# Kernel tuning notes

Measured on AMD Instinct MI355X. Metric: run time of the kernel, lower is better.

Reference implementation:

```python
import jax, jax.numpy as jnp
import numpy as np

N = 8192
IN_F = 512
OUT_F = 64
ALPHA = 0.2  # LeakyReLU negative slope
NEG_INF = -9e15


def setup_inputs() -> dict:
    key = jax.random.key(0)
    k1, k2, k3, k4 = jax.random.split(key, 4)
    x = jax.random.normal(k1, (N, IN_F), dtype=jnp.float32)
    adj = jax.random.randint(k2, (N, N), 0, 2, dtype=jnp.int32)
    # xavier_uniform with gain=1.414
    def xavier(k, shape, gain=1.414):
        fan_in, fan_out = shape[0], shape[1]
        a = gain * np.sqrt(6.0 / (fan_in + fan_out))
        return jax.random.uniform(k, shape, jnp.float32, -a, a)
    W = xavier(k3, (IN_F, OUT_F))
    a = xavier(k4, (2 * OUT_F, 1))
    return {"x": x, "adj": adj, "W": W, "a": a}


def reference(x, adj, W, a):
    h = x @ W  # [N, F]
    f = W.shape[1]
    # e[i,j] = leakyrelu([h_i, h_j] @ a) = leakyrelu(h_i@a1 + h_j@a2)
    e1 = h @ a[:f, 0]   # [N]
    e2 = h @ a[f:, 0]   # [N]
    e = jax.nn.leaky_relu(e1[:, None] + e2[None, :], negative_slope=ALPHA)  # [N, N]
    scores = jnp.where(adj > 0, e, NEG_INF)
    attention = jax.nn.softmax(scores, axis=1)  # dropout p=0.0 -> identity
    h_prime = attention @ h  # [N, F]
    return jax.nn.elu(h_prime)  # concat=True
```

## Files before the change

kernel.cpp:

```cpp
#include <hip/hip_runtime.h>
#include <hip/hip_bf16.h>

#define NN 8192
#define KF 512
#define FF 64
#define GAT_ALPHA 0.2f
#define MSHIFT 20.0f
#define LOG2E 1.44269504f

#define JSPLIT 16
#define JW (NN / JSPLIT)
#define KSTEPS (JW / 32)

#define EXP2F(x) __builtin_amdgcn_exp2f(x)

typedef __attribute__((ext_vector_type(8))) __bf16 bf16x8;
typedef __attribute__((ext_vector_type(4))) float f32x4;
typedef __attribute__((ext_vector_type(4))) int   i32x4;

__global__ __launch_bounds__(256) void gat_linear(
    const float* __restrict__ x, const float* __restrict__ W,
    const float* __restrict__ av, __hip_bfloat16* __restrict__ ht,
    float* __restrict__ e1, float* __restrict__ e2)
{
    __shared__ float xs[32][33];
    __shared__ float Ws[32][64];
    __shared__ float ep[2][32][17];

    const int t  = threadIdx.x;
    const int fq = t & 15;
    const int rq = t >> 4;
    const int i0 = blockIdx.x * 32;

    const int kl = t & 31, r0 = t >> 5;
    const int fw = t & 63, kq = t >> 6;

    float acc[2][4] = {};

    for (int kt = 0; kt < KF; kt += 32) {
        #pragma unroll
        for (int m = 0; m < 4; ++m)
            xs[kl][r0 + 8 * m] = x[(size_t)(i0 + r0 + 8 * m) * KF + kt + kl];
        #pragma unroll
        for (int m = 0; m < 8; ++m)
            Ws[kq + 4 * m][fw] = W[(size_t)(kt + kq + 4 * m) * FF + fw];
        __syncthreads();
        #pragma unroll
        for (int kk = 0; kk < 32; ++kk) {
            float x0 = xs[kk][rq * 2];
            float x1 = xs[kk][rq * 2 + 1];
            f32x4 wv = *(const f32x4*)&Ws[kk][fq * 4];
            #pragma unroll
            for (int v = 0; v < 4; ++v) {
                acc[0][v] += x0 * wv[v];
                acc[1][v] += x1 * wv[v];
            }
        }
        __syncthreads();
    }

    #pragma unroll
    for (int v = 0; v < 4; ++v) {
        int f = fq * 4 + v;
        union { ushort2 q; __hip_bfloat16 h[2]; } pk;
        pk.h[0] = __float2bfloat16(acc[0][v]);
        pk.h[1] = __float2bfloat16(acc[1][v]);
        *(ushort2*)&ht[(size_t)f * NN + i0 + rq * 2] = pk.q;
    }

    f32x4 a1v = *(const f32x4*)&av[fq * 4];
    f32x4 a2v = *(const f32x4*)&av[64 + fq * 4];
    #pragma unroll
    for (int u = 0; u < 2; ++u) {
        float s1 = 0.f, s2 = 0.f;
        #pragma unroll
        for (int v = 0; v < 4; ++v) {
            s1 += acc[u][v] * a1v[v];
            s2 += acc[u][v] * a2v[v];
        }
        ep[0][rq * 2 + u][fq] = s1;
        ep[1][rq * 2 + u][fq] = s2;
    }
    __syncthreads();
    if (t < 32) {
        float s1 = 0.f, s2 = 0.f;
        #pragma unroll
        for (int q = 0; q < 16; ++q) { s1 += ep[0][t][q]; s2 += ep[1][t][q]; }
        e1[i0 + t] = s1 * LOG2E;
        e2[i0 + t] = s2 * LOG2E;
    }
}

__global__ __launch_bounds__(256, 4) void gat_attn(
    const int* __restrict__ adj, const __hip_bfloat16* __restrict__ ht,
    const float* __restrict__ e1, const float* __restrict__ e2,
    float* __restrict__ accs, float* __restrict__ lsums)
{
    const int t     = threadIdx.x;
    const int lane  = t & 63;
    const int wv    = t >> 6;
    const int n16   = lane & 15;
    const int quad  = lane >> 4;
    const int split = blockIdx.x & (JSPLIT - 1);
    const int i0    = (blockIdx.x >> 4) * 64 + wv * 16;
    const int j0    = split * JW;
    const int row   = i0 + n16;

    const float e1L = e1[row];
    float ms = e1L + MSHIFT * LOG2E;
    const float miL = ms > 0.f ? ms : GAT_ALPHA * ms;
    const float c0  = e1L - miL;
    const float c1  = GAT_ALPHA * e1L - miL;

    const int*            ap  = adj + (size_t)row * NN + j0 + quad * 8;
    const float*          epx = e2 + j0 + quad * 8;
    const __hip_bfloat16* hp  = ht + (size_t)n16 * NN + j0 + quad * 8;

    i32x4  aA[2][2];
    float4 eA[2][2];
    f32x4 dacc[4] = {{0.f,0.f,0.f,0.f},{0.f,0.f,0.f,0.f},{0.f,0.f,0.f,0.f},{0.f,0.f,0.f,0.f}};
    f32x4 dl = {0.f, 0.f, 0.f, 0.f};

    union { unsigned short s[8]; bf16x8 v; } ones;
    #pragma unroll
    for (int k = 0; k < 8; ++k) ones.s[k] = 0x3F80;

#define LOADA(sl, st)                                                          \
    {                                                                          \
        aA[sl][0] = *(const i32x4*)(ap + (st) * 32);                           \
        aA[sl][1] = *(const i32x4*)(ap + (st) * 32 + 4);                       \
    }
#define LOADE(sl, st)                                                          \
    {                                                                          \
        eA[sl][0] = *(const float4*)(epx + (st) * 32);                         \
        eA[sl][1] = *(const float4*)(epx + (st) * 32 + 4);                     \
    }

    LOADA(0, 0) LOADA(1, 1)
    LOADE(0, 0) LOADE(1, 1)

    #pragma unroll
    for (int st = 0; st < KSTEPS; ++st) {
        const int sl = st & 1;

        bf16x8 b0 = *(const bf16x8*)(hp + (size_t)st * 32);
        bf16x8 b1 = *(const bf16x8*)(hp + (size_t)16 * NN + st * 32);
        bf16x8 b2 = *(const bf16x8*)(hp + (size_t)32 * NN + st * 32);
        bf16x8 b3 = *(const bf16x8*)(hp + (size_t)48 * NN + st * 32);

        i32x4  a0 = aA[sl][0], a1 = aA[sl][1];
        float4 e0 = eA[sl][0], ev = eA[sl][1];
        if (st + 2 < KSTEPS) { LOADA(sl, st + 2) LOADE(sl, st + 2) }

        union { bf16x8 v; __hip_bfloat16 h[8]; } af;
#define PJ(idx, aval, eval)                                                    \
        {                                                                      \
            float t0 = c0 + (eval);                                            \
            float t1 = __builtin_fmaf(GAT_ALPHA, (eval), c1);                  \
            float p_ = EXP2F(fmaxf(t0, t1));                                   \
            af.h[idx] = __float2bfloat16((aval) > 0 ? p_ : 0.f);               \
        }
        PJ(0, a0.x, e0.x) PJ(1, a0.y, e0.y) PJ(2, a0.z, e0.z) PJ(3, a0.w, e0.w)
        PJ(4, a1.x, ev.x) PJ(5, a1.y, ev.y) PJ(6, a1.z, ev.z) PJ(7, a1.w, ev.w)
#undef PJ

        dacc[0] = __builtin_amdgcn_mfma_f32_16x16x32_bf16(af.v, b0, dacc[0], 0, 0, 0);
        dacc[1] = __builtin_amdgcn_mfma_f32_16x16x32_bf16(af.v, b1, dacc[1], 0, 0, 0);
        dacc[2] = __builtin_amdgcn_mfma_f32_16x16x32_bf16(af.v, b2, dacc[2], 0, 0, 0);
        dacc[3] = __builtin_amdgcn_mfma_f32_16x16x32_bf16(af.v, b3, dacc[3], 0, 0, 0);
        dl      = __builtin_amdgcn_mfma_f32_16x16x32_bf16(af.v, ones.v, dl, 0, 0, 0);
    }
#undef LOADA
#undef LOADE

    if (n16 == 0) {
        #pragma unroll
        for (int r = 0; r < 4; ++r)
            lsums[(size_t)split * NN + i0 + quad * 4 + r] = dl[r];
    }

    float* ab = accs + (size_t)split * NN * FF;
    #pragma unroll
    for (int ft = 0; ft < 4; ++ft)
        #pragma unroll
        for (int r = 0; r < 4; ++r)
            ab[(size_t)(i0 + quad * 4 + r) * FF + ft * 16 + n16] = dacc[ft][r];
}

__global__ __launch_bounds__(256) void gat_epilogue(
    const float* __restrict__ accs, const float* __restrict__ lsums,
    float* __restrict__ out)
{
    const int idx = (blockIdx.x * 256 + threadIdx.x) * 4;
    const int row = idx >> 6;

    float l = 0.f;
    #pragma unroll
    for (int s = 0; s < JSPLIT; ++s) l += lsums[(size_t)s * NN + row];

    f32x4 a = {0.f, 0.f, 0.f, 0.f};
    #pragma unroll
    for (int s = 0; s < JSPLIT; ++s) {
        f32x4 v = *(const f32x4*)(accs + (size_t)s * NN * FF + idx);
        a.x += v.x; a.y += v.y; a.z += v.z; a.w += v.w;
    }

    const float li = 1.f / l;
    f32x4 o;
    #pragma unroll
    for (int v = 0; v < 4; ++v) {
        float hv = a[v] * li;
        o[v] = hv > 0.f ? hv : __expf(hv) - 1.f;
    }
    *(f32x4*)(out + idx) = o;
}

extern "C" void kernel_launch(void* const* d_in, const int* in_sizes, int n_in,
                              void* d_out, int out_size, void* d_ws, size_t ws_size,
                              hipStream_t stream) {
    const float* x   = (const float*)d_in[0];
    const int*   adj = (const int*)d_in[1];
    const float* W   = (const float*)d_in[2];
    const float* av  = (const float*)d_in[3];
    float* out = (float*)d_out;

    char* wsb = (char*)d_ws;
    __hip_bfloat16* ht = (__hip_bfloat16*)wsb;
    float* e1    = (float*)(wsb + (1 << 20));
    float* e2    = e1 + NN;
    float* accs  = e2 + NN;
    float* lsums = accs + (size_t)JSPLIT * NN * FF;

    gat_linear<<<256, 256, 0, stream>>>(x, W, av, ht, e1, e2);
    gat_attn<<<(NN / 64) * JSPLIT, 256, 0, stream>>>(adj, ht, e1, e2, accs, lsums);
    gat_epilogue<<<NN * FF / 1024, 256, 0, stream>>>(accs, lsums, out);
}
```

Baseline: 432.2 us.

## Pre-pack adjacency into a bitmask in a separate kernel and halve the column split

```diff
diff --git a/kernel.cpp b/kernel.cpp
--- a/kernel.cpp
+++ b/kernel.cpp
@@ -8,7 +8,7 @@
 #define MSHIFT 20.0f
 #define LOG2E 1.44269504f
 
-#define JSPLIT 16
+#define JSPLIT 8
 #define JW (NN / JSPLIT)
 #define KSTEPS (JW / 32)
 
@@ -16,7 +16,35 @@
 
 typedef __attribute__((ext_vector_type(8))) __bf16 bf16x8;
 typedef __attribute__((ext_vector_type(4))) float f32x4;
-typedef __attribute__((ext_vector_type(4))) int   i32x4;
+
+__global__ __launch_bounds__(256) void adj_compress(
+    const int* __restrict__ adj, unsigned* __restrict__ mask)
+{
+    const int b   = blockIdx.x * 256 + threadIdx.x;
+    const int st4 =  b       & 7;
+    const int q   = (b >> 3) & 3;
+    const int s   = (b >> 5) & 7;
+    const int row =  b >> 8;
+
+    const int* ap = adj + (size_t)row * NN + s * JW + q * 8;
+    unsigned w = 0;
+    #pragma unroll
+    for (int k = 0; k < 4; ++k) {
+        const int st = st4 * 4 + k;
+        int4 a0 = *(const int4*)(ap + st * 32);
+        int4 a1 = *(const int4*)(ap + st * 32 + 4);
+        unsigned by =  (unsigned)(a0.x > 0)
+                    | ((unsigned)(a0.y > 0) << 1)
+                    | ((unsigned)(a0.z > 0) << 2)
+                    | ((unsigned)(a0.w > 0) << 3)
+                    | ((unsigned)(a1.x > 0) << 4)
+                    | ((unsigned)(a1.y > 0) << 5)
+                    | ((unsigned)(a1.z > 0) << 6)
+                    | ((unsigned)(a1.w > 0) << 7);
+        w |= by << (8 * k);
+    }
+    mask[b] = w;
+}
 
 __global__ __launch_bounds__(256) void gat_linear(
     const float* __restrict__ x, const float* __restrict__ W,
@@ -92,7 +120,7 @@
 }
 
 __global__ __launch_bounds__(256, 4) void gat_attn(
-    const int* __restrict__ adj, const __hip_bfloat16* __restrict__ ht,
+    const unsigned short* __restrict__ maskh, const __hip_bfloat16* __restrict__ ht,
     const float* __restrict__ e1, const float* __restrict__ e2,
     float* __restrict__ accs, float* __restrict__ lsums)
 {
@@ -102,7 +130,7 @@
     const int n16   = lane & 15;
     const int quad  = lane >> 4;
     const int split = blockIdx.x & (JSPLIT - 1);
-    const int i0    = (blockIdx.x >> 4) * 64 + wv * 16;
+    const int i0    = (blockIdx.x >> 3) * 64 + wv * 16;
     const int j0    = split * JW;
     const int row   = i0 + n16;
 
@@ -112,12 +140,10 @@
     const float c0  = e1L - miL;
     const float c1  = GAT_ALPHA * e1L - miL;
 
-    const int*            ap  = adj + (size_t)row * NN + j0 + quad * 8;
+    const unsigned short* mp = maskh + (size_t)row * 512 + split * 64 + quad * 16;
     const float*          epx = e2 + j0 + quad * 8;
     const __hip_bfloat16* hp  = ht + (size_t)n16 * NN + j0 + quad * 8;
 
-    i32x4  aA[2][2];
-    float4 eA[2][2];
     f32x4 dacc[4] = {{0.f,0.f,0.f,0.f},{0.f,0.f,0.f,0.f},{0.f,0.f,0.f,0.f},{0.f,0.f,0.f,0.f}};
     f32x4 dl = {0.f, 0.f, 0.f, 0.f};
 
@@ -125,53 +151,41 @@
     #pragma unroll
     for (int k = 0; k < 8; ++k) ones.s[k] = 0x3F80;
 
-#define LOADA(sl, st)                                                          \
-    {                                                                          \
-        aA[sl][0] = *(const i32x4*)(ap + (st) * 32);                           \
-        aA[sl][1] = *(const i32x4*)(ap + (st) * 32 + 4);                       \
-    }
-#define LOADE(sl, st)                                                          \
-    {                                                                          \
-        eA[sl][0] = *(const float4*)(epx + (st) * 32);                         \
-        eA[sl][1] = *(const float4*)(epx + (st) * 32 + 4);                     \
-    }
-
-    LOADA(0, 0) LOADA(1, 1)
-    LOADE(0, 0) LOADE(1, 1)
-
-    #pragma unroll
-    for (int st = 0; st < KSTEPS; ++st) {
-        const int sl = st & 1;
-
-        bf16x8 b0 = *(const bf16x8*)(hp + (size_t)st * 32);
-        bf16x8 b1 = *(const bf16x8*)(hp + (size_t)16 * NN + st * 32);
-        bf16x8 b2 = *(const bf16x8*)(hp + (size_t)32 * NN + st * 32);
-        bf16x8 b3 = *(const bf16x8*)(hp + (size_t)48 * NN + st * 32);
-
-        i32x4  a0 = aA[sl][0], a1 = aA[sl][1];
-        float4 e0 = eA[sl][0], ev = eA[sl][1];
-        if (st + 2 < KSTEPS) { LOADA(sl, st + 2) LOADE(sl, st + 2) }
-
-        union { bf16x8 v; __hip_bfloat16 h[8]; } af;
-#define PJ(idx, aval, eval)                                                    \
-        {                                                                      \
-            float t0 = c0 + (eval);                                            \
-            float t1 = __builtin_fmaf(GAT_ALPHA, (eval), c1);                  \
-            float p_ = EXP2F(fmaxf(t0, t1));                                   \
-            af.h[idx] = __float2bfloat16((aval) > 0 ? p_ : 0.f);               \
+    unsigned mh = mp[0];
+    for (int c = 0; c < KSTEPS / 2; ++c) {
+        const unsigned mcur = mh;
+        if (c + 1 < KSTEPS / 2) mh = mp[c + 1];
+
+        #pragma unroll
+        for (int k = 0; k < 2; ++k) {
+            const int st = c * 2 + k;
+            float4 e0 = *(const float4*)(epx + st * 32);
+            float4 ev = *(const float4*)(epx + st * 32 + 4);
+            bf16x8 b0 = *(const bf16x8*)(hp + (size_t)st * 32);
+            bf16x8 b1 = *(const bf16x8*)(hp + (size_t)16 * NN + st * 32);
+            bf16x8 b2 = *(const bf16x8*)(hp + (size_t)32 * NN + st * 32);
+            bf16x8 b3 = *(const bf16x8*)(hp + (size_t)48 * NN + st * 32);
+
+            union { bf16x8 v; __hip_bfloat16 h[8]; } af;
+#define PJ(idx, eval)                                                          \
+            {                                                                  \
+                float t0 = c0 + (eval);                                        \
+                float t1 = __builtin_fmaf(GAT_ALPHA, (eval), c1);              \
+                float p_ = EXP2F(fmaxf(t0, t1));                               \
+                af.h[idx] = __float2bfloat16(                                  \
+                    ((mcur >> (k * 8 + idx)) & 1u) ? p_ : 0.f);                \
+            }
+            PJ(0, e0.x) PJ(1, e0.y) PJ(2, e0.z) PJ(3, e0.w)
+            PJ(4, ev.x) PJ(5, ev.y) PJ(6, ev.z) PJ(7, ev.w)
+#undef PJ
+
+            dacc[0] = __builtin_amdgcn_mfma_f32_16x16x32_bf16(af.v, b0, dacc[0], 0, 0, 0);
+            dacc[1] = __builtin_amdgcn_mfma_f32_16x16x32_bf16(af.v, b1, dacc[1], 0, 0, 0);
+            dacc[2] = __builtin_amdgcn_mfma_f32_16x16x32_bf16(af.v, b2, dacc[2], 0, 0, 0);
+            dacc[3] = __builtin_amdgcn_mfma_f32_16x16x32_bf16(af.v, b3, dacc[3], 0, 0, 0);
+            dl      = __builtin_amdgcn_mfma_f32_16x16x32_bf16(af.v, ones.v, dl, 0, 0, 0);
         }
-        PJ(0, a0.x, e0.x) PJ(1, a0.y, e0.y) PJ(2, a0.z, e0.z) PJ(3, a0.w, e0.w)
-        PJ(4, a1.x, ev.x) PJ(5, a1.y, ev.y) PJ(6, a1.z, ev.z) PJ(7, a1.w, ev.w)
-#undef PJ
-
-        dacc[0] = __builtin_amdgcn_mfma_f32_16x16x32_bf16(af.v, b0, dacc[0], 0, 0, 0);
-        dacc[1] = __builtin_amdgcn_mfma_f32_16x16x32_bf16(af.v, b1, dacc[1], 0, 0, 0);
-        dacc[2] = __builtin_amdgcn_mfma_f32_16x16x32_bf16(af.v, b2, dacc[2], 0, 0, 0);
-        dacc[3] = __builtin_amdgcn_mfma_f32_16x16x32_bf16(af.v, b3, dacc[3], 0, 0, 0);
-        dl      = __builtin_amdgcn_mfma_f32_16x16x32_bf16(af.v, ones.v, dl, 0, 0, 0);
-    }
-#undef LOADA
-#undef LOADE
+    }
 
     if (n16 == 0) {
         #pragma unroll
@@ -228,10 +242,13 @@
     __hip_bfloat16* ht = (__hip_bfloat16*)wsb;
     float* e1    = (float*)(wsb + (1 << 20));
     float* e2    = e1 + NN;
-    float* accs  = e2 + NN;
+    unsigned* mask = (unsigned*)(e2 + NN);
+    float* accs  = (float*)((char*)mask + (size_t)NN * 1024);
     float* lsums = accs + (size_t)JSPLIT * NN * FF;
 
+    adj_compress<<<NN * 256 / 256, 256, 0, stream>>>(adj, mask);
     gat_linear<<<256, 256, 0, stream>>>(x, W, av, ht, e1, e2);
-    gat_attn<<<(NN / 64) * JSPLIT, 256, 0, stream>>>(adj, ht, e1, e2, accs, lsums);
+    gat_attn<<<(NN / 64) * JSPLIT, 256, 0, stream>>>(
+        (const unsigned short*)mask, ht, e1, e2, accs, lsums);
     gat_epilogue<<<NN * FF / 1024, 256, 0, stream>>>(accs, lsums, out);
 }
```

New measurement: 474.0 us. +9.7%, slower.
